# Performance work log

Measured on AMD Instinct MI355X. Metric: run time of the kernel, lower is better.

Reference implementation:

```python
import jax, jax.numpy as jnp
import numpy as np

V = 50257   # vocab_size
D = 768     # d_model
NL = 4      # n_layers
DI = 1536   # d_inner = expand * d_model
DS = 16     # d_state
DC = 4      # d_conv
B = 2       # batch
L = 512     # seq_len
EPS = 1e-5  # RMSNorm eps
STD = 0.02  # init std


def setup_inputs() -> dict:
    key = jax.random.key(0)
    ks = jax.random.split(key, 8)
    idx = jax.random.randint(ks[0], (B, L), 0, V)
    emb = jax.random.normal(ks[1], (V, D), dtype=jnp.float32) * STD          # tied embedding / lm_head
    W_in = jax.random.normal(ks[2], (NL, 2 * DI, D), dtype=jnp.float32) * STD
    conv_w = jax.random.normal(ks[3], (NL, DI, 1, DC), dtype=jnp.float32) * STD  # depthwise conv [O,I/g,K]
    W_xproj = jax.random.normal(ks[4], (NL, 2 * DS + 1, DI), dtype=jnp.float32) * STD
    W_dt = jax.random.normal(ks[5], (NL, DI, 1), dtype=jnp.float32) * STD    # dt_rank = 1
    b_dt = jnp.zeros((NL, DI), dtype=jnp.float32)
    a_log = jnp.tile(jnp.log(jnp.arange(1, DS + 1, dtype=jnp.float32)), (NL, DI, 1))
    d_param = jnp.ones((NL, DI), dtype=jnp.float32)
    W_out = jax.random.normal(ks[6], (NL, D, DI), dtype=jnp.float32) * STD
    norm_w = jnp.ones((D,), dtype=jnp.float32)
    return dict(idx=idx, emb=emb, W_in=W_in, conv_w=conv_w, W_xproj=W_xproj,
                W_dt=W_dt, b_dt=b_dt, a_log=a_log, d_param=d_param,
                W_out=W_out, norm_w=norm_w)


def _mamba_block(x, W_in, conv_w, W_xproj, W_dt, b_dt, a_log, d_param, W_out):
    # in_proj + split into x, z
    xz = jnp.einsum('bld,ed->ble', x, W_in)            # [B,L,2*DI]
    xs, z = jnp.split(xz, 2, axis=-1)
    # causal depthwise conv1d (torch pads d_conv-1 both sides, keeps first L -> left pad only)
    xc = jnp.transpose(xs, (0, 2, 1))                  # [B,DI,L]
    xc = jax.lax.conv_general_dilated(xc, conv_w, window_strides=(1,),
                                      padding=[(DC - 1, 0)],
                                      feature_group_count=DI,
                                      dimension_numbers=('NCH', 'OIH', 'NCH'))
    xs = jax.nn.silu(jnp.transpose(xc, (0, 2, 1)))     # [B,L,DI]
    # selective SSM
    A = -jnp.exp(a_log)                                # [DI,DS]
    xp = jnp.einsum('bld,ed->ble', xs, W_xproj)        # [B,L,2*DS+1]
    dt_raw = xp[..., 0]                                # [B,L]
    Bp = xp[..., 1:1 + DS]                             # [B,L,DS]
    Cp = xp[..., 1 + DS:]                              # [B,L,DS]
    delta = jax.nn.softplus(dt_raw[..., None] * W_dt[:, 0] + b_dt)  # [B,L,DI]

    def step(h, inp):
        d_i, b_i, c_i, x_i = inp                       # [B,DI],[B,DS],[B,DS],[B,DI]
        a_bar = jnp.exp(d_i[:, :, None] * A)           # [B,DI,DS]
        h = a_bar * h + d_i[:, :, None] * b_i[:, None, :] * x_i[:, :, None]
        y = jnp.einsum('bn,bdn->bd', c_i, h) + d_param * x_i
        return h, y

    h0 = jnp.zeros((x.shape[0], DI, DS), dtype=x.dtype)
    seq = (jnp.moveaxis(delta, 1, 0), jnp.moveaxis(Bp, 1, 0),
           jnp.moveaxis(Cp, 1, 0), jnp.moveaxis(xs, 1, 0))
    _, ys = jax.lax.scan(step, h0, seq)
    y = jnp.moveaxis(ys, 0, 1)                         # [B,L,DI]
    y = y * jax.nn.silu(z)
    return jnp.einsum('ble,de->bld', y, W_out)         # [B,L,D]


def reference(idx, emb, W_in, conv_w, W_xproj, W_dt, b_dt, a_log, d_param, W_out, norm_w):
    x = emb[idx]                                       # [B,L,D]

    def layer(carry, p):
        w_in, c_w, w_xp, w_dt, bdt, alog, dpar, w_out = p
        out = carry + _mamba_block(carry, w_in, c_w, w_xp, w_dt, bdt, alog, dpar, w_out)
        return out, None

    x, _ = jax.lax.scan(layer, x, (W_in, conv_w, W_xproj, W_dt, b_dt, a_log, d_param, W_out))
    rms = jax.lax.rsqrt(jnp.mean(x * x, axis=-1, keepdims=True) + EPS)
    x = x * rms * norm_w
    logits = jnp.einsum('bld,vd->blv', x, emb)         # tied lm_head
    return logits
```

## Files before the change

### kernel.cpp

```cpp
#include <hip/hip_runtime.h>
#include <cstdint>

#define VV     50257
#define VPAD   50432
#define DMODEL 768
#define NLAYER 4
#define DINNER 1536
#define DSTATE 16
#define DCONV  4
#define BATCH  2
#define SEQ    512
#define MROWS  (BATCH*SEQ)

typedef unsigned short u16;
typedef __attribute__((ext_vector_type(8))) short bf16x8;
typedef __attribute__((ext_vector_type(4))) float f32x4;

__device__ __forceinline__ u16 f2bf(float f) {
  unsigned u = __float_as_uint(f);
  u += 0x7fffu + ((u >> 16) & 1u);
  return (u16)(u >> 16);
}

__device__ __forceinline__ void async16(const void* g, void* l) {
  auto gp = reinterpret_cast<const __attribute__((address_space(1))) unsigned int*>(
      reinterpret_cast<uintptr_t>(g));
  auto lp = reinterpret_cast<__attribute__((address_space(3))) unsigned int*>(
      reinterpret_cast<uintptr_t>(l));
  __builtin_amdgcn_global_load_lds(gp, lp, 16, 0, 0);
}

__global__ void prep_kern(const float* __restrict__ emb, const float* __restrict__ W_in,
                          const float* __restrict__ W_out, const int* __restrict__ idx,
                          u16* __restrict__ embbf, u16* __restrict__ winbf,
                          u16* __restrict__ woutbf, float* __restrict__ xf,
                          u16* __restrict__ xbf) {
  const int E4  = VPAD * DMODEL / 4;
  const int W14 = NLAYER * 2 * DINNER * DMODEL / 4;
  const int W24 = NLAYER * DMODEL * DINNER / 4;
  const int X4  = MROWS * DMODEL / 4;
  const int TOT = E4 + W14 + W24 + X4;
  int i = blockIdx.x * blockDim.x + threadIdx.x;
  const int stride = gridDim.x * blockDim.x;
  for (; i < TOT; i += stride) {
    if (i < E4) {
      ushort4 o;
      if (i < VV * DMODEL / 4) {
        float4 v = *(const float4*)(emb + (long)i * 4);
        o.x = f2bf(v.x); o.y = f2bf(v.y); o.z = f2bf(v.z); o.w = f2bf(v.w);
      } else { o.x = 0; o.y = 0; o.z = 0; o.w = 0; }
      *(ushort4*)(embbf + (long)i * 4) = o;
    } else if (i < E4 + W14) {
      const int j = i - E4;
      float4 v = *(const float4*)(W_in + (long)j * 4);
      ushort4 o; o.x = f2bf(v.x); o.y = f2bf(v.y); o.z = f2bf(v.z); o.w = f2bf(v.w);
      *(ushort4*)(winbf + (long)j * 4) = o;
    } else if (i < E4 + W14 + W24) {
      const int j = i - E4 - W14;
      float4 v = *(const float4*)(W_out + (long)j * 4);
      ushort4 o; o.x = f2bf(v.x); o.y = f2bf(v.y); o.z = f2bf(v.z); o.w = f2bf(v.w);
      *(ushort4*)(woutbf + (long)j * 4) = o;
    } else {
      const int j = i - E4 - W14 - W24;
      const int r = j / (DMODEL / 4);
      const int c = (j % (DMODEL / 4)) * 4;
      const int id = idx[r];
      float4 v = *(const float4*)(emb + (long)id * DMODEL + c);
      *(float4*)(xf + (long)r * DMODEL + c) = v;
      ushort4 o; o.x = f2bf(v.x); o.y = f2bf(v.y); o.z = f2bf(v.z); o.w = f2bf(v.w);
      *(ushort4*)(xbf + (long)r * DMODEL + c) = o;
    }
  }
}

template<bool GUARDN, bool XSWZ>
__global__ __launch_bounds__(256) void gemm3_kern(
    const u16* __restrict__ A, const u16* __restrict__ B,
    float* __restrict__ C, int M, int N, int K, int lda, int ldb)
{
  __shared__ u16 As[3][128 * 32];
  __shared__ u16 Bs[3][128 * 32];
  int bx, by;
  if (XSWZ) {
    const int nt = gridDim.x >> 3;
    const int t = (blockIdx.x & 7) * nt + (blockIdx.x >> 3);
    bx = t & 7; by = t >> 3;
  } else { bx = blockIdx.x; by = blockIdx.y; }
  const int koff = blockIdx.z * K;
  const long coff = (long)blockIdx.z * M * N;

  const int tid  = threadIdx.x;
  const int wave = tid >> 6;
  const int lane = tid & 63;
  const int wr = wave >> 1, wc = wave & 1;
  const int m0 = bx * 128;
  const int n0 = by * 128;

  const int srow = wave * 32 + (lane >> 2);
  const int sblk = ((lane & 3) ^ ((lane >> 3) & 3)) * 8;

  f32x4 acc[4][4];
#pragma unroll
  for (int i = 0; i < 4; ++i)
#pragma unroll
    for (int j = 0; j < 4; ++j) acc[i][j] = (f32x4){0.f, 0.f, 0.f, 0.f};

  const int arow = wr * 64 + (lane & 15);
  const int brow = wc * 64 + (lane & 15);
  const int sa   = (((lane >> 4) ^ ((lane >> 1) & 3)) << 3);

  const int KT = K / 32;
  auto stage = [&](int kt) {
    const int slot = kt % 3;
    const long kcol = (long)koff + kt * 32;
#pragma unroll
    for (int j = 0; j < 2; ++j) {
      async16(A + (long)(m0 + srow + j * 16) * lda + kcol + sblk,
              (char*)(As[slot]) + (wave * 32 + j * 16) * 64);
      async16(B + (long)(n0 + srow + j * 16) * ldb + kcol + sblk,
              (char*)(Bs[slot]) + (wave * 32 + j * 16) * 64);
    }
  };

  stage(0);
  stage(1);
  for (int t = 0; t < KT; ++t) {
    if (t + 2 < KT) {
      stage(t + 2);
      asm volatile("s_waitcnt vmcnt(8)" ::: "memory");
    } else if (t + 2 == KT) {
      asm volatile("s_waitcnt vmcnt(4)" ::: "memory");
    } else {
      asm volatile("s_waitcnt vmcnt(0)" ::: "memory");
    }
    __builtin_amdgcn_s_barrier();
    asm volatile("" ::: "memory");

    const int slot = t % 3;
    const u16* as = As[slot];
    const u16* bs = Bs[slot];
    bf16x8 af[4], bv[4];
#pragma unroll
    for (int i = 0; i < 4; ++i) af[i] = *(const bf16x8*)(as + (arow + 16 * i) * 32 + sa);
#pragma unroll
    for (int j = 0; j < 4; ++j) bv[j] = *(const bf16x8*)(bs + (brow + 16 * j) * 32 + sa);

    __builtin_amdgcn_s_setprio(1);
#pragma unroll
    for (int i = 0; i < 4; ++i)
#pragma unroll
      for (int j = 0; j < 4; ++j)
        acc[i][j] = __builtin_amdgcn_mfma_f32_16x16x32_bf16(af[i], bv[j], acc[i][j], 0, 0, 0);
    __builtin_amdgcn_s_setprio(0);

    asm volatile("" ::: "memory");
    __builtin_amdgcn_s_barrier();
    asm volatile("" ::: "memory");
  }

  const int rbase = m0 + wr * 64 + ((lane >> 4) << 2);
  const int cbase = n0 + wc * 64 + (lane & 15);
#pragma unroll
  for (int j = 0; j < 4; ++j) {
    const int col = cbase + j * 16;
    if (GUARDN && col >= N) continue;
#pragma unroll
    for (int i = 0; i < 4; ++i) {
#pragma unroll
      for (int r = 0; r < 4; ++r) {
        const int row = rbase + i * 16 + r;
        C[coff + (long)row * N + col] = acc[i][j][r];
      }
    }
  }
}

__global__ __launch_bounds__(512, 2) void gemm8_kern(
    const u16* __restrict__ A, const u16* __restrict__ B,
    float* __restrict__ C, int N, int K, int lda, int ldb)
{
  __shared__ u16 lds[2][2][256 * 64];
  const int tid = threadIdx.x;
  const int wave = tid >> 6;
  const int lane = tid & 63;
  const int wm = wave >> 2, wn = wave & 3;

  const int nwg = gridDim.x;
  const int q = nwg >> 3, r = nwg & 7;
  const int xcd = blockIdx.x & 7;
  const int t = (xcd < r ? xcd * (q + 1) : r * (q + 1) + (xcd - r) * q) + (blockIdx.x >> 3);
  const int m0 = (t & 3) * 256;
  const int n0 = (t >> 2) * 256;

  const int NT = K / 64;
  const int NI = NT / 2;

  const int sblk = (((lane & 7) ^ (lane >> 3)) << 3);
  auto stage = [&](int buf, int ab, int half, int kt) {
    const u16* Mat = ab ? B : A;
    const int ld = ab ? ldb : lda;
    const int tb = ab ? n0 : m0;
#pragma unroll
    for (int j = 0; j < 2; ++j) {
      const int rloc = half * 128 + j * 64 + wave * 8;
      async16(Mat + (long)(tb + rloc + (lane >> 3)) * ld + kt * 64 + sblk,
              (char*)&lds[buf][ab][0] + (rloc << 7));
    }
  };

  bf16x8 af[4][2], bl[2][2], bh[2][2];
  const int aq = lane >> 4;
  auto readA = [&](int buf, int half) {
#pragma unroll
    for (int mf = 0; mf < 4; ++mf) {
      const int rr = half * 128 + wm * 64 + mf * 16 + (lane & 15);
#pragma unroll
      for (int ks = 0; ks < 2; ++ks) {
        const int q2 = ks * 4 + aq;
        af[mf][ks] = *(const bf16x8*)(&lds[buf][0][0] + rr * 64 + ((q2 ^ (rr & 7)) << 3));
      }
    }
  };
  auto readB = [&](int buf, int half, bf16x8 (&bf)[2][2]) {
#pragma unroll
    for (int nf = 0; nf < 2; ++nf) {
      const int rr = half * 128 + wn * 32 + nf * 16 + (lane & 15);
#pragma unroll
      for (int ks = 0; ks < 2; ++ks) {
        const int q2 = ks * 4 + aq;
        bf[nf][ks] = *(const bf16x8*)(&lds[buf][1][0] + rr * 64 + ((q2 ^ (rr & 7)) << 3));
      }
    }
  };

  f32x4 acc[8][4];
#pragma unroll
  for (int i = 0; i < 8; ++i)
#pragma unroll
    for (int j = 0; j < 4; ++j) acc[i][j] = (f32x4){0.f, 0.f, 0.f, 0.f};

#define MFMA16(QM, QN, BF)                                                        \
  __builtin_amdgcn_s_setprio(1);                                                  \
  _Pragma("unroll")                                                               \
  for (int mf = 0; mf < 4; ++mf)                                                  \
    _Pragma("unroll")                                                             \
    for (int nf = 0; nf < 2; ++nf)                                                \
      _Pragma("unroll")                                                           \
      for (int ks = 0; ks < 2; ++ks)                                              \
        acc[(QM)*4+mf][(QN)*2+nf] = __builtin_amdgcn_mfma_f32_16x16x32_bf16(      \
            af[mf][ks], BF[nf][ks], acc[(QM)*4+mf][(QN)*2+nf], 0, 0, 0);          \
  __builtin_amdgcn_s_setprio(0);

#define BAR()  asm volatile("" ::: "memory"); __builtin_amdgcn_s_barrier(); asm volatile("" ::: "memory")
#define LGKM0() asm volatile("s_waitcnt lgkmcnt(0)" ::: "memory")

  stage(0, 0, 0, 0); stage(0, 1, 0, 0); stage(0, 1, 1, 0);
  stage(0, 0, 1, 0); stage(1, 0, 0, 1); stage(1, 1, 0, 1);
  asm volatile("s_waitcnt vmcnt(8)" ::: "memory");
  BAR();

  for (int it = 0; it < NI; ++it) {
    const int kt = it * 2;
    const bool last = (it == NI - 1);
    readA(0, 0); readB(0, 0, bl);
    stage(1, 0, 1, kt + 1);
    asm volatile("s_waitcnt vmcnt(6)" ::: "memory");
    BAR(); LGKM0();
    MFMA16(0, 0, bl);
    BAR();
    readB(0, 1, bh);
    stage(1, 1, 1, kt + 1);
    BAR(); LGKM0();
    MFMA16(0, 1, bh);
    BAR();
    readA(0, 1);
    if (!last) stage(0, 0, 0, kt + 2);
    BAR(); LGKM0();
    MFMA16(1, 0, bl);
    BAR();
    if (!last) { stage(0, 1, 0, kt + 2);
      asm volatile("s_waitcnt vmcnt(8)" ::: "memory");
    } else {
      asm volatile("s_waitcnt vmcnt(4)" ::: "memory");
    }
    BAR();
    MFMA16(1, 1, bh);
    BAR();
    readA(1, 0); readB(1, 0, bl);
    if (!last) { stage(0, 0, 1, kt + 2);
      asm volatile("s_waitcnt vmcnt(6)" ::: "memory");
    } else {
      asm volatile("s_waitcnt vmcnt(0)" ::: "memory");
    }
    BAR(); LGKM0();
    MFMA16(0, 0, bl);
    BAR();
    readB(1, 1, bh);
    if (!last) stage(0, 1, 1, kt + 2);
    BAR(); LGKM0();
    MFMA16(0, 1, bh);
    BAR();
    readA(1, 1);
    if (!last) stage(1, 0, 0, kt + 3);
    BAR(); LGKM0();
    MFMA16(1, 0, bl);
    BAR();
    if (!last) { stage(1, 1, 0, kt + 3);
      asm volatile("s_waitcnt vmcnt(8)" ::: "memory");
    }
    BAR();
    MFMA16(1, 1, bh);
    if (!last) { BAR(); }
  }

#pragma unroll
  for (int qm = 0; qm < 2; ++qm)
#pragma unroll
    for (int mf = 0; mf < 4; ++mf)
#pragma unroll
      for (int qn = 0; qn < 2; ++qn)
#pragma unroll
        for (int nf = 0; nf < 2; ++nf) {
          const int col = n0 + qn * 128 + wn * 32 + nf * 16 + (lane & 15);
          if (col >= N) continue;
          const int row0 = m0 + qm * 128 + wm * 64 + mf * 16 + ((lane >> 4) << 2);
          const f32x4 v = acc[qm * 4 + mf][qn * 2 + nf];
#pragma unroll
          for (int rr2 = 0; rr2 < 4; ++rr2)
            C[(long)(row0 + rr2) * N + col] = v[rr2];
        }
#undef MFMA16
#undef BAR
#undef LGKM0
}

__global__ __launch_bounds__(256) void redout_kern(const float* __restrict__ part,
                                                   float* __restrict__ xf,
                                                   u16* __restrict__ xbf) {
  const int i = blockIdx.x * blockDim.x + threadIdx.x;
  if (i >= MROWS * DMODEL / 4) return;
  const int stride4 = MROWS * DMODEL / 4;
  float4 s = ((const float4*)part)[i];
  float4 p1 = ((const float4*)part)[i + stride4];
  float4 p2 = ((const float4*)part)[i + 2 * stride4];
  float4 p3 = ((const float4*)part)[i + 3 * stride4];
  float4 x = ((const float4*)xf)[i];
  s.x += p1.x + p2.x + p3.x + x.x;
  s.y += p1.y + p2.y + p3.y + x.y;
  s.z += p1.z + p2.z + p3.z + x.z;
  s.w += p1.w + p2.w + p3.w + x.w;
  ((float4*)xf)[i] = s;
  ushort4 o; o.x = f2bf(s.x); o.y = f2bf(s.y); o.z = f2bf(s.z); o.w = f2bf(s.w);
  ((ushort4*)xbf)[i] = o;
}

__global__ __launch_bounds__(256) void convxproj_kern(
    const float* __restrict__ xz, const float* __restrict__ cw,
    const float* __restrict__ Wx, const float* __restrict__ wdt,
    const float* __restrict__ bdt,
    float* __restrict__ xs, float* __restrict__ dlt, float* __restrict__ bc)
{
  __shared__ float sx[DINNER];
  __shared__ float sxp[40];
  const int row = blockIdx.x;
  const int t = row & (SEQ - 1);
  const int tid = threadIdx.x;

  for (int c = tid; c < DINNER; c += 256) {
    const float* w = cw + c * DCONV;
    float a = 0.f;
#pragma unroll
    for (int k = 0; k < DCONV; ++k) {
      const int tt = t - (DCONV - 1) + k;
      if (tt >= 0) a += w[k] * xz[(long)(row - (DCONV - 1) + k) * (2 * DINNER) + c];
    }
    const float s = a / (1.f + __expf(-a));
    sx[c] = s;
    xs[(long)row * DINNER + c] = s;
  }
  __syncthreads();

  const int wv = tid >> 6, lane = tid & 63;
  for (int e = wv; e < 2 * DSTATE + 1; e += 4) {
    const float* We = Wx + (long)e * DINNER;
    float p = 0.f;
    for (int d = lane; d < DINNER; d += 64) p += sx[d] * We[d];
#pragma unroll
    for (int off = 32; off; off >>= 1) p += __shfl_xor(p, off, 64);
    if (lane == 0) sxp[e] = p;
  }
  __syncthreads();
  const float dtr = sxp[0];
  for (int d = tid; d < DINNER; d += 256) {
    float v = dtr * wdt[d] + bdt[d];
    float sp = (v > 15.f) ? v : log1pf(__expf(v));
    dlt[(long)row * DINNER + d] = sp;
  }
  if (tid < 2 * DSTATE) bc[(long)row * (2 * DSTATE) + tid] = sxp[1 + tid];
}

__global__ __launch_bounds__(128) void scan_kern(
    const float* __restrict__ dlt, const float* __restrict__ bc,
    const float* __restrict__ xs, const float* __restrict__ xz,
    const float* __restrict__ alog, const float* __restrict__ dpar,
    u16* __restrict__ ybf)
{
  __shared__ float sh_h[16][8][DSTATE];
  __shared__ float sh_s[16][8];
  const int tid = threadIdx.x;
  const int ch = tid & 7, chunk = tid >> 3;
  const int ch_abs = blockIdx.x * 8 + ch;
  const int b = ch_abs / DINNER, d = ch_abs % DINNER;
  float An[DSTATE];
#pragma unroll
  for (int n = 0; n < DSTATE; ++n) An[n] = -__expf(alog[(long)d * DSTATE + n]);
  const int r0 = b * SEQ + chunk * 32;

  float h[DSTATE];
#pragma unroll
  for (int n = 0; n < DSTATE; ++n) h[n] = 0.f;
  float ssum = 0.f;
  for (int s = 0; s < 32; ++s) {
    const int row = r0 + s;
    const float dl = dlt[(long)row * DINNER + d];
    const float xv = xs[(long)row * DINNER + d];
    const float dx = dl * xv;
    const float4* bp = (const float4*)(bc + (long)row * (2 * DSTATE));
    float Bv[DSTATE];
    *(float4*)&Bv[0]  = bp[0]; *(float4*)&Bv[4]  = bp[1];
    *(float4*)&Bv[8]  = bp[2]; *(float4*)&Bv[12] = bp[3];
    ssum += dl;
#pragma unroll
    for (int n = 0; n < DSTATE; ++n) h[n] = __expf(dl * An[n]) * h[n] + dx * Bv[n];
  }
#pragma unroll
  for (int n = 0; n < DSTATE; ++n) sh_h[chunk][ch][n] = h[n];
  sh_s[chunk][ch] = ssum;
  __syncthreads();

  {
    const int n2 = tid & 15, ch2 = tid >> 4;
    const int d2 = (blockIdx.x * 8 + ch2) % DINNER;
    const float A2 = -__expf(alog[(long)d2 * DSTATE + n2]);
    float carry = 0.f;
    for (int c = 0; c < 16; ++c) {
      const float hl = sh_h[c][ch2][n2];
      sh_h[c][ch2][n2] = carry;
      carry = __expf(A2 * sh_s[c][ch2]) * carry + hl;
    }
  }
  __syncthreads();

#pragma unroll
  for (int n = 0; n < DSTATE; ++n) h[n] = sh_h[chunk][ch][n];
  const float dp = dpar[d];
  for (int s = 0; s < 32; ++s) {
    const int row = r0 + s;
    const float dl = dlt[(long)row * DINNER + d];
    const float xv = xs[(long)row * DINNER + d];
    const float dx = dl * xv;
    const float4* bp = (const float4*)(bc + (long)row * (2 * DSTATE));
    float Bv[DSTATE], Cv[DSTATE];
    *(float4*)&Bv[0]  = bp[0]; *(float4*)&Bv[4]  = bp[1];
    *(float4*)&Bv[8]  = bp[2]; *(float4*)&Bv[12] = bp[3];
    *(float4*)&Cv[0]  = bp[4]; *(float4*)&Cv[4]  = bp[5];
    *(float4*)&Cv[8]  = bp[6]; *(float4*)&Cv[12] = bp[7];
    float y = 0.f;
#pragma unroll
    for (int n = 0; n < DSTATE; ++n) {
      const float hn = __expf(dl * An[n]) * h[n] + dx * Bv[n];
      h[n] = hn;
      y += Cv[n] * hn;
    }
    y += dp * xv;
    const float zz = xz[(long)row * (2 * DINNER) + DINNER + d];
    const float o = y * (zz / (1.f + __expf(-zz)));
    ybf[(long)row * DINNER + d] = f2bf(o);
  }
}

__global__ __launch_bounds__(256) void rmsnorm_kern(const float* __restrict__ x,
                                                    const float* __restrict__ nw,
                                                    u16* __restrict__ xnbf) {
  const int row = blockIdx.x, tid = threadIdx.x;
  const float* xr = x + (long)row * DMODEL;
  float p = 0.f;
#pragma unroll
  for (int k = 0; k < 3; ++k) { float v = xr[tid + k * 256]; p += v * v; }
#pragma unroll
  for (int off = 32; off; off >>= 1) p += __shfl_xor(p, off, 64);
  __shared__ float red[4];
  __shared__ float s_rms;
  const int wv = tid >> 6, lane = tid & 63;
  if (lane == 0) red[wv] = p;
  __syncthreads();
  if (tid == 0) {
    float tsum = red[0] + red[1] + red[2] + red[3];
    s_rms = rsqrtf(tsum / (float)DMODEL + 1e-5f);
  }
  __syncthreads();
  const float r = s_rms;
#pragma unroll
  for (int k = 0; k < 3; ++k) {
    const int dd = tid + k * 256;
    xnbf[(long)row * DMODEL + dd] = f2bf(xr[dd] * r * nw[dd]);
  }
}

extern "C" void kernel_launch(void* const* d_in, const int* in_sizes, int n_in,
                              void* d_out, int out_size, void* d_ws, size_t ws_size,
                              hipStream_t stream)
{
  (void)in_sizes; (void)n_in; (void)out_size; (void)ws_size;
  const int*   idx   = (const int*)  d_in[0];
  const float* emb   = (const float*)d_in[1];
  const float* W_in  = (const float*)d_in[2];
  const float* convw = (const float*)d_in[3];
  const float* W_xp  = (const float*)d_in[4];
  const float* W_dt  = (const float*)d_in[5];
  const float* b_dt  = (const float*)d_in[6];
  const float* a_log = (const float*)d_in[7];
  const float* d_par = (const float*)d_in[8];
  const float* W_out = (const float*)d_in[9];
  const float* normw = (const float*)d_in[10];
  float* out = (float*)d_out;

  char* ws = (char*)d_ws;
  size_t off = 0;
  auto alloc = [&](size_t bytes) -> void* {
    void* p = ws + off;
    off += (bytes + 255) & ~(size_t)255;
    return p;
  };
  u16*   embbf  = (u16*)  alloc((size_t)VPAD * DMODEL * 2);
  u16*   winbf  = (u16*)  alloc((size_t)NLAYER * 2 * DINNER * DMODEL * 2);
  u16*   woutbf = (u16*)  alloc((size_t)NLAYER * DMODEL * DINNER * 2);
  float* xf     = (float*)alloc((size_t)MROWS * DMODEL * 4);
  u16*   xbf    = (u16*)  alloc((size_t)MROWS * DMODEL * 2);
  float* xz     = (float*)alloc((size_t)MROWS * 2 * DINNER * 4);
  float* xs     = (float*)alloc((size_t)MROWS * DINNER * 4);
  float* dlt    = (float*)alloc((size_t)MROWS * DINNER * 4);
  float* bc     = (float*)alloc((size_t)MROWS * 2 * DSTATE * 4);
  u16*   ybf    = (u16*)  alloc((size_t)MROWS * DINNER * 2);
  u16*   xnbf   = (u16*)  alloc((size_t)MROWS * DMODEL * 2);
  float* part   = (float*)alloc((size_t)4 * MROWS * DMODEL * 4);

  prep_kern<<<2048, 256, 0, stream>>>(emb, W_in, W_out, idx, embbf, winbf, woutbf, xf, xbf);

  for (int l = 0; l < NLAYER; ++l) {
    gemm3_kern<false, true><<<8 * (2 * DINNER / 128), 256, 0, stream>>>(
        xbf, winbf + (size_t)l * 2 * DINNER * DMODEL, xz,
        MROWS, 2 * DINNER, DMODEL, DMODEL, DMODEL);
    convxproj_kern<<<MROWS, 256, 0, stream>>>(
        xz, convw + (size_t)l * DINNER * DCONV,
        W_xp + (size_t)l * (2 * DSTATE + 1) * DINNER,
        W_dt + (size_t)l * DINNER, b_dt + (size_t)l * DINNER, xs, dlt, bc);
    scan_kern<<<BATCH * DINNER / 8, 128, 0, stream>>>(
        dlt, bc, xs, xz, a_log + (size_t)l * DINNER * DSTATE, d_par + (size_t)l * DINNER, ybf);
    gemm3_kern<false, true><<<dim3(8 * (DMODEL / 128), 1, 4), 256, 0, stream>>>(
        ybf, woutbf + (size_t)l * DMODEL * DINNER, part,
        MROWS, DMODEL, DINNER / 4, DINNER, DINNER);
    redout_kern<<<MROWS * DMODEL / 4 / 256, 256, 0, stream>>>(part, xf, xbf);
  }
  rmsnorm_kern<<<MROWS, 256, 0, stream>>>(xf, normw, xnbf);
  gemm8_kern<<<4 * (VPAD / 256), 512, 0, stream>>>(
      xnbf, embbf, out, VV, DMODEL, DMODEL, DMODEL);
}
```

Baseline: 896.3 us.

## Restructure lm_head GEMM pipeline and fuse final residual reduce into RMSNorm

```diff
diff --git a/kernel.cpp b/kernel.cpp
--- a/kernel.cpp
+++ b/kernel.cpp
@@ -193,7 +193,6 @@
   const int n0 = (t >> 2) * 256;
 
   const int NT = K / 64;
-  const int NI = NT / 2;
 
   const int sblk = (((lane & 7) ^ (lane >> 3)) << 3);
   auto stage = [&](int buf, int ab, int half, int kt) {
@@ -251,66 +250,51 @@
             af[mf][ks], BF[nf][ks], acc[(QM)*4+mf][(QN)*2+nf], 0, 0, 0);          \
   __builtin_amdgcn_s_setprio(0);
 
-#define BAR()  asm volatile("" ::: "memory"); __builtin_amdgcn_s_barrier(); asm volatile("" ::: "memory")
-#define LGKM0() asm volatile("s_waitcnt lgkmcnt(0)" ::: "memory")
-
-  stage(0, 0, 0, 0); stage(0, 1, 0, 0); stage(0, 1, 1, 0);
-  stage(0, 0, 1, 0); stage(1, 0, 0, 1); stage(1, 1, 0, 1);
-  asm volatile("s_waitcnt vmcnt(8)" ::: "memory");
+#define BAR()   asm volatile("" ::: "memory"); __builtin_amdgcn_s_barrier(); asm volatile("" ::: "memory")
+#define WAITV(N) asm volatile("s_waitcnt vmcnt(" #N ")" ::: "memory"); __builtin_amdgcn_sched_barrier(0)
+#define WAITL(N) asm volatile("s_waitcnt lgkmcnt(" #N ")" ::: "memory"); __builtin_amdgcn_sched_barrier(0)
+
+  stage(0, 0, 0, 0); stage(0, 1, 0, 0); stage(0, 1, 1, 0); stage(0, 0, 1, 0);
+  stage(1, 0, 0, 1); stage(1, 1, 0, 1); stage(1, 1, 1, 1);
+  WAITV(6);
   BAR();
-
-  for (int it = 0; it < NI; ++it) {
-    const int kt = it * 2;
-    const bool last = (it == NI - 1);
-    readA(0, 0); readB(0, 0, bl);
-    stage(1, 0, 1, kt + 1);
-    asm volatile("s_waitcnt vmcnt(6)" ::: "memory");
-    BAR(); LGKM0();
-    MFMA16(0, 0, bl);
-    BAR();
-    readB(0, 1, bh);
-    stage(1, 1, 1, kt + 1);
-    BAR(); LGKM0();
-    MFMA16(0, 1, bh);
-    BAR();
-    readA(0, 1);
-    if (!last) stage(0, 0, 0, kt + 2);
-    BAR(); LGKM0();
-    MFMA16(1, 0, bl);
-    BAR();
-    if (!last) { stage(0, 1, 0, kt + 2);
-      asm volatile("s_waitcnt vmcnt(8)" ::: "memory");
-    } else {
-      asm volatile("s_waitcnt vmcnt(4)" ::: "memory");
-    }
-    BAR();
-    MFMA16(1, 1, bh);
-    BAR();
-    readA(1, 0); readB(1, 0, bl);
-    if (!last) { stage(0, 0, 1, kt + 2);
-      asm volatile("s_waitcnt vmcnt(6)" ::: "memory");
-    } else {
-      asm volatile("s_waitcnt vmcnt(0)" ::: "memory");
-    }
-    BAR(); LGKM0();
-    MFMA16(0, 0, bl);
-    BAR();
-    readB(1, 1, bh);
-    if (!last) stage(0, 1, 1, kt + 2);
-    BAR(); LGKM0();
-    MFMA16(0, 1, bh);
-    BAR();
-    readA(1, 1);
-    if (!last) stage(1, 0, 0, kt + 3);
-    BAR(); LGKM0();
-    MFMA16(1, 0, bl);
-    BAR();
-    if (!last) { stage(1, 1, 0, kt + 3);
-      asm volatile("s_waitcnt vmcnt(8)" ::: "memory");
-    }
-    BAR();
-    MFMA16(1, 1, bh);
-    if (!last) { BAR(); }
+  readB(0, 0, bl);
+
+#define TILE(KTE, BUF)                                                            \
+  {                                                                               \
+    const int kt = (KTE);                                                         \
+                                                               \
+    if (kt >= NT - 2) { WAITV(0); } else { WAITV(8); }                            \
+    BAR();                                                                        \
+    readA(BUF, 0);                                          \
+    readB(BUF, 1, bh);                            \
+    if (kt + 1 < NT) stage(BUF ^ 1, 0, 1, kt + 1);                  \
+    WAITL(4);                                  \
+    MFMA16(0, 0, bl);                                                             \
+                                                               \
+    BAR();                                                                        \
+    if (kt + 2 < NT) stage(BUF, 0, 0, kt + 2);                      \
+    WAITL(0);                                                      \
+    MFMA16(0, 1, bh);                                                             \
+                                                               \
+    if (kt >= NT - 2) { WAITV(0); } else { WAITV(10); }                           \
+    BAR();                                                                        \
+    readA(BUF, 1);                           \
+    if (kt + 2 < NT) stage(BUF, 1, 0, kt + 2);                      \
+    WAITL(0);                                                     \
+    MFMA16(1, 0, bl);                                                             \
+                                                               \
+    if (kt >= NT - 2) { WAITV(0); } else { WAITV(8); }                            \
+    BAR();                                                                        \
+    if (kt + 1 < NT) readB(BUF ^ 1, 0, bl);               \
+    if (kt + 2 < NT) stage(BUF, 1, 1, kt + 2);                      \
+    WAITL(4);                                      \
+    MFMA16(1, 1, bh);                                                             \
+  }
+
+  for (int kt2 = 0; kt2 < NT; kt2 += 2) {
+    TILE(kt2, 0);
+    TILE(kt2 + 1, 1);
   }
 
 #pragma unroll
@@ -329,9 +313,11 @@
           for (int rr2 = 0; rr2 < 4; ++rr2)
             C[(long)(row0 + rr2) * N + col] = v[rr2];
         }
+#undef TILE
 #undef MFMA16
 #undef BAR
-#undef LGKM0
+#undef WAITV
+#undef WAITL
 }
 
 __global__ __launch_bounds__(256) void redout_kern(const float* __restrict__ part,
@@ -479,14 +465,21 @@
   }
 }
 
-__global__ __launch_bounds__(256) void rmsnorm_kern(const float* __restrict__ x,
+__global__ __launch_bounds__(256) void rmsfuse_kern(const float* __restrict__ part,
+                                                    const float* __restrict__ xf,
                                                     const float* __restrict__ nw,
                                                     u16* __restrict__ xnbf) {
   const int row = blockIdx.x, tid = threadIdx.x;
-  const float* xr = x + (long)row * DMODEL;
+  const int S = MROWS * DMODEL;
+  float v[3];
   float p = 0.f;
 #pragma unroll
-  for (int k = 0; k < 3; ++k) { float v = xr[tid + k * 256]; p += v * v; }
+  for (int k = 0; k < 3; ++k) {
+    const int i = row * DMODEL + tid + k * 256;
+    float x = xf[i] + part[i] + part[i + S] + part[i + 2 * S] + part[i + 3 * S];
+    v[k] = x;
+    p += x * x;
+  }
 #pragma unroll
   for (int off = 32; off; off >>= 1) p += __shfl_xor(p, off, 64);
   __shared__ float red[4];
@@ -503,7 +496,7 @@
 #pragma unroll
   for (int k = 0; k < 3; ++k) {
     const int dd = tid + k * 256;
-    xnbf[(long)row * DMODEL + dd] = f2bf(xr[dd] * r * nw[dd]);
+    xnbf[(long)row * DMODEL + dd] = f2bf(v[k] * r * nw[dd]);
   }
 }
 
@@ -560,9 +553,10 @@
     gemm3_kern<false, true><<<dim3(8 * (DMODEL / 128), 1, 4), 256, 0, stream>>>(
         ybf, woutbf + (size_t)l * DMODEL * DINNER, part,
         MROWS, DMODEL, DINNER / 4, DINNER, DINNER);
-    redout_kern<<<MROWS * DMODEL / 4 / 256, 256, 0, stream>>>(part, xf, xbf);
-  }
-  rmsnorm_kern<<<MROWS, 256, 0, stream>>>(xf, normw, xnbf);
+    if (l < NLAYER - 1)
+      redout_kern<<<MROWS * DMODEL / 4 / 256, 256, 0, stream>>>(part, xf, xbf);
+  }
+  rmsfuse_kern<<<MROWS, 256, 0, stream>>>(part, xf, normw, xnbf);
   gemm8_kern<<<4 * (VPAD / 256), 512, 0, stream>>>(
       xnbf, embbf, out, VV, DMODEL, DMODEL, DMODEL);
 }
```

Measured after the change: 883.5 us. No clear change (-1.4%).
